# Performance work log

Hardware: AMD Instinct MI355X
Metric: run time of the kernel (lower is better)

Reference implementation:

```python
import jax, jax.numpy as jnp
import numpy as np

B, C, D, H, W = 2, 96, 4, 128, 128
WS = 8            # spatial window size
NUM_HEADS = 3
MLP_RATIO = 4.0


def _rel_pos_index(ws_eff):
    # Swin-style 2D relative position index over the effective (ws*sqrt(D))^2 window
    coords = np.stack(np.meshgrid(np.arange(ws_eff), np.arange(ws_eff), indexing='ij')).reshape(2, -1)
    rel = (coords[:, :, None] - coords[:, None, :]).transpose(1, 2, 0)
    rel[..., 0] += ws_eff - 1
    rel[..., 1] += ws_eff - 1
    rel[..., 0] *= 2 * ws_eff - 1
    return rel.sum(-1)  # (N, N) int


def setup_inputs() -> dict:
    key = jax.random.key(0)
    ks = jax.random.split(key, 8)
    ws_eff = WS * int(np.sqrt(D))
    table_len = (2 * ws_eff - 1) ** 2
    hid = int(C * MLP_RATIO)
    s = lambda k, shape: jax.random.normal(k, shape, jnp.float32) * 0.02
    return dict(
        x=jax.random.normal(ks[0], (B, C, D, H, W), jnp.float32),
        qkv_w=s(ks[1], (3 * C, C)), qkv_b=jnp.zeros((3 * C,), jnp.float32),
        proj_w=s(ks[2], (C, C)), proj_b=jnp.zeros((C,), jnp.float32),
        bias_table=s(ks[3], (table_len, NUM_HEADS)),
        ln1_g=jnp.ones((C,), jnp.float32), ln1_b=jnp.zeros((C,), jnp.float32),
        ln2_g=jnp.ones((C,), jnp.float32), ln2_b=jnp.zeros((C,), jnp.float32),
        fc1_w=s(ks[4], (hid, C)), fc1_b=jnp.zeros((hid,), jnp.float32),
        fc2_w=s(ks[5], (C, hid)), fc2_b=jnp.zeros((C,), jnp.float32),
    )


def _ln(x, g, b):
    m = x.mean(-1, keepdims=True)
    v = ((x - m) ** 2).mean(-1, keepdims=True)
    return (x - m) * jax.lax.rsqrt(v + 1e-5) * g + b


def reference(x, qkv_w, qkv_b, proj_w, proj_b, bias_table,
              ln1_g, ln1_b, ln2_g, ln2_b, fc1_w, fc1_b, fc2_w, fc2_b):
    ws, nh = WS, NUM_HEADS
    hd = C // nh
    # window partition: (B,C,D,H,W) -> (nW*B, C, D*ws*ws) -> tokens (B_, N, C)
    p = x.reshape(B, C, D, H // ws, ws, W // ws, ws)
    p = p.transpose(0, 3, 5, 1, 2, 4, 6).reshape(-1, C, D * ws * ws)
    t = p.transpose(0, 2, 1)  # (B_, N, C)
    B_, N, _ = t.shape

    # --- window attention with relative position bias ---
    h = _ln(t, ln1_g, ln1_b)
    qkv = (h @ qkv_w.T + qkv_b).reshape(B_, N, 3, nh, hd).transpose(2, 0, 3, 1, 4)
    q = qkv[0] * (hd ** -0.5)
    k, v = qkv[1], qkv[2]
    idx = jnp.asarray(_rel_pos_index(ws * int(np.sqrt(D))))  # static (N,N)
    bias = bias_table[idx].transpose(2, 0, 1)  # (nh, N, N) gathered bias
    attn = jax.nn.softmax(jnp.einsum('bhnd,bhmd->bhnm', q, k) + bias[None], axis=-1)
    o = jnp.einsum('bhnm,bhmd->bhnd', attn, v).transpose(0, 2, 1, 3).reshape(B_, N, C)
    t = t + (o @ proj_w.T + proj_b)

    # --- MLP block ---
    h2 = _ln(t, ln2_g, ln2_b)
    m = jax.nn.gelu(h2 @ fc1_w.T + fc1_b, approximate=False) @ fc2_w.T + fc2_b
    return t + m
```

## Files before the change

kernel.cpp:

```cpp
#include <hip/hip_runtime.h>
#include <hip/hip_bf16.h>

typedef unsigned int u32;
typedef unsigned long long u64;
using bf16x8 = __attribute__((ext_vector_type(8))) short;
using f32x4  = __attribute__((ext_vector_type(4))) float;

#define QKV_STRIDE 12582912u
#define WS_NEED    100663296ull

__device__ __forceinline__ float bl(u32 u) { return __uint_as_float(u << 16); }
__device__ __forceinline__ float bh(u32 u) { return __uint_as_float(u & 0xffff0000u); }
__device__ __forceinline__ unsigned short bfbits(float f) {
    __hip_bfloat16 b = __float2bfloat16(f);
    return *(unsigned short*)&b;
}
__device__ __forceinline__ u32 pack2(float f0, float f1) {
    return ((u32)bfbits(f1) << 16) | (u32)bfbits(f0);
}
__device__ __forceinline__ u64 pack4(float f0, float f1, float f2, float f3) {
    return ((u64)pack2(f2, f3) << 32) | (u64)pack2(f0, f1);
}

#define MFMA(a, b, c) __builtin_amdgcn_mfma_f32_16x16x32_bf16(a, b, c, 0, 0, 0)

__global__ __launch_bounds__(256) void k_fill(float* __restrict__ out, int n)
{
    int i = blockIdx.x * 256 + threadIdx.x;
    if (i < n) out[i] = 1000.0f;
}

__global__ __launch_bounds__(256) void k_ln1_c(const float* __restrict__ x,
                                               const float* __restrict__ g1,
                                               const float* __restrict__ b1,
                                               u32* __restrict__ h)
{
    __shared__ float xs[96 * 128];
    __shared__ float ps[256], pss[256], mr[128], rs[128];
    int blk = blockIdx.x;
    int hh = blk & 127, d = (blk >> 7) & 3, bb = blk >> 9;
    long base = (long)bb * 6291456 + (long)d * 16384 + hh * 128;
    for (int i = threadIdx.x; i < 3072; i += 256) {
        int c = i >> 5, w4 = i & 31;
        ((float4*)xs)[i] = *(const float4*)(x + base + (long)c * 65536 + w4 * 4);
    }
    __syncthreads();

    int tid = threadIdx.x, half = tid >> 7, ww = tid & 127;
    int c0 = half * 48;
    float s = 0.f, ssq = 0.f;
    #pragma unroll 8
    for (int c = c0; c < c0 + 48; ++c) {
        float v = xs[c * 128 + ww];
        s += v; ssq += v * v;
    }
    ps[tid] = s; pss[tid] = ssq;
    __syncthreads();
    if (half == 0) {
        float st = ps[ww] + ps[128 + ww], sst = pss[ww] + pss[128 + ww];
        float mean = st * (1.f / 96.f);
        float var  = sst * (1.f / 96.f) - mean * mean;
        mr[ww] = mean; rs[ww] = rsqrtf(var + 1e-5f);
    }
    __syncthreads();
    float mean = mr[ww], rstd = rs[ww];

    int w = (bb << 8) + (hh >> 3) * 16 + (ww >> 3);
    int t = (w << 8) + d * 64 + (hh & 7) * 8 + (ww & 7);
    uint4* hq = (uint4*)(h + (long)t * 48 + half * 24);
    #pragma unroll
    for (int k = 0; k < 6; ++k) {
        int c = c0 + 8 * k;
        u32 q0 = pack2((xs[(c+0)*128+ww]-mean)*rstd*g1[c+0]+b1[c+0],
                       (xs[(c+1)*128+ww]-mean)*rstd*g1[c+1]+b1[c+1]);
        u32 q1 = pack2((xs[(c+2)*128+ww]-mean)*rstd*g1[c+2]+b1[c+2],
                       (xs[(c+3)*128+ww]-mean)*rstd*g1[c+3]+b1[c+3]);
        u32 q2 = pack2((xs[(c+4)*128+ww]-mean)*rstd*g1[c+4]+b1[c+4],
                       (xs[(c+5)*128+ww]-mean)*rstd*g1[c+5]+b1[c+5]);
        u32 q3 = pack2((xs[(c+6)*128+ww]-mean)*rstd*g1[c+6]+b1[c+6],
                       (xs[(c+7)*128+ww]-mean)*rstd*g1[c+7]+b1[c+7]);
        hq[k] = make_uint4(q0, q1, q2, q3);
    }
}

__global__ __launch_bounds__(256) void k_qkv_m(const __hip_bfloat16* __restrict__ h,
                                               const float* __restrict__ qkvw,
                                               const float* __restrict__ qkvb,
                                               __hip_bfloat16* __restrict__ qkv)
{
    __shared__ short wsm[288 * 96];
    int tid = threadIdx.x;
    for (int idx = tid; idx < 6912; idx += 256) {
        float4 wv = ((const float4*)qkvw)[idx];
        *(u64*)&wsm[idx * 4] = pack4(wv.x, wv.y, wv.z, wv.w);
    }
    __syncthreads();

    int wave = tid >> 6, lane = tid & 63;
    int quad = lane >> 4, l16 = lane & 15;
    int mbase = blockIdx.x * 256 + wave * 64;

    bf16x8 A[4][3];
    #pragma unroll
    for (int mm = 0; mm < 4; ++mm) {
        const __hip_bfloat16* ap = h + (long)(mbase + mm * 16 + l16) * 96 + quad * 8;
        A[mm][0] = *(const bf16x8*)(ap);
        A[mm][1] = *(const bf16x8*)(ap + 32);
        A[mm][2] = *(const bf16x8*)(ap + 64);
    }

    for (int nt = 0; nt < 18; ++nt) {
        int n0 = nt * 16;
        const short* bp = &wsm[(n0 + l16) * 96 + quad * 8];
        bf16x8 B0 = *(const bf16x8*)(bp);
        bf16x8 B1 = *(const bf16x8*)(bp + 32);
        bf16x8 B2 = *(const bf16x8*)(bp + 64);
        int r    = n0 + l16;
        int type = n0 / 96;
        int head = (n0 % 96) / 32;
        int dd   = r & 31;
        float bias = qkvb[r];
        float scl  = (type == 0) ? 0.17677669529663687f : 1.0f;
        long tbase = (long)type * QKV_STRIDE;
        #pragma unroll
        for (int mm = 0; mm < 4; ++mm) {
            f32x4 acc = {0.f, 0.f, 0.f, 0.f};
            acc = MFMA(A[mm][0], B0, acc);
            acc = MFMA(A[mm][1], B1, acc);
            acc = MFMA(A[mm][2], B2, acc);
            int tok0 = mbase + mm * 16 + quad * 4;
            int w = tok0 >> 8, nn = tok0 & 255;
            long dst0 = tbase + (long)(w * 3 + head) * 8192 + nn * 32 + dd;
            #pragma unroll
            for (int rg = 0; rg < 4; ++rg)
                qkv[dst0 + (long)rg * 32] = __float2bfloat16((acc[rg] + bias) * scl);
        }
    }
}

__global__ __launch_bounds__(256, 6) void k_attn_m(const __hip_bfloat16* __restrict__ qkv,
                                                   const float* __restrict__ btab,
                                                   __hip_bfloat16* __restrict__ o)
{
    __shared__ short vt[32 * 264];
    __shared__ float bsT[31 * 33];
    int wh = blockIdx.x, head = wh % 3, w = wh / 3;
    int tid = threadIdx.x;

    const u32* vg = (const u32*)(qkv + 2u * QKV_STRIDE + (long)wh * 8192);
    for (int idx = tid; idx < 4096; idx += 256) {
        u32 pv = vg[idx];
        int kr = idx >> 4, d0 = (idx & 15) * 2;
        vt[d0 * 264 + kr]       = (short)(pv & 0xffffu);
        vt[(d0 + 1) * 264 + kr] = (short)(pv >> 16);
    }
    for (int idx = tid; idx < 961; idx += 256) {
        int c2 = idx / 31, r2 = idx - c2 * 31;
        bsT[c2 * 33 + r2] = btab[(r2 * 31 + c2) * 3 + head];
    }
    __syncthreads();

    int wave = tid >> 6, lane = tid & 63, quad = lane >> 4, l16 = lane & 15;
    const __hip_bfloat16* qb = qkv + (long)wh * 8192;
    const __hip_bfloat16* kb = qkv + QKV_STRIDE + (long)wh * 8192;

    int addrA = ((((lane >> 4) & 1) << 5) + l16) << 2;
    int addrB = addrA + 64;
    int addrI = (quad * 20) << 2;
    bool hiq  = (quad >= 2);

    #pragma unroll 1
    for (int g = 0; g < 4; ++g) {
        int qg = wave * 4 + g;
        bf16x8 qf = *(const bf16x8*)(qb + (qg * 16 + l16) * 32 + quad * 8);
        f32x4 a0 = {0.f, 0.f, 0.f, 0.f}, a1 = {0.f, 0.f, 0.f, 0.f};
        float lsum = 0.f;

        #pragma unroll 1
        for (int qt = 0; qt < 4; ++qt) {
            f32x4 s[4];
            #pragma unroll
            for (int k4 = 0; k4 < 4; ++k4) {
                int kt = qt * 4 + k4;
                bf16x8 kkv = *(const bf16x8*)(kb + (kt * 16 + l16) * 32 + quad * 8);
                f32x4 z = {0.f, 0.f, 0.f, 0.f};
                s[k4] = MFMA(kkv, qf, z);
            }
            #pragma unroll
            for (int rg = 0; rg < 4; ++rg) {
                const float* bb = &bsT[(l16 - quad * 4 + 15 - rg) * 33 + qg];
                #pragma unroll
                for (int k4 = 0; k4 < 4; ++k4)
                    s[k4][rg] += bb[15 - qt * 4 - k4];
            }
            f32x4 vs = {0.f, 0.f, 0.f, 0.f};
            #pragma unroll
            for (int k4 = 0; k4 < 4; ++k4) {
                f32x4 e;
                #pragma unroll
                for (int rg = 0; rg < 4; ++rg) e[rg] = __expf(s[k4][rg]);
                s[k4] = e;
                vs += e;
            }
            lsum += vs[0] + vs[1] + vs[2] + vs[3];

            #pragma unroll
            for (int k2l = 0; k2l < 2; ++k2l) {
                int k2 = qt * 2 + k2l;
                u32 pe0 = pack2(s[2 * k2l][0],     s[2 * k2l][1]);
                u32 pe1 = pack2(s[2 * k2l][2],     s[2 * k2l][3]);
                u32 po0 = pack2(s[2 * k2l + 1][0], s[2 * k2l + 1][1]);
                u32 po1 = pack2(s[2 * k2l + 1][2], s[2 * k2l + 1][3]);
                u32 e0 = (u32)__builtin_amdgcn_ds_bpermute(addrA, (int)pe0);
                u32 o0 = (u32)__builtin_amdgcn_ds_bpermute(addrA, (int)po0);
                u32 e1 = (u32)__builtin_amdgcn_ds_bpermute(addrA, (int)pe1);
                u32 o1 = (u32)__builtin_amdgcn_ds_bpermute(addrA, (int)po1);
                u32 e2 = (u32)__builtin_amdgcn_ds_bpermute(addrB, (int)pe0);
                u32 o2 = (u32)__builtin_amdgcn_ds_bpermute(addrB, (int)po0);
                u32 e3 = (u32)__builtin_amdgcn_ds_bpermute(addrB, (int)pe1);
                u32 o3 = (u32)__builtin_amdgcn_ds_bpermute(addrB, (int)po1);
                union { u32 u[4]; bf16x8 v; } pu;
                pu.u[0] = hiq ? o0 : e0;
                pu.u[1] = hiq ? o1 : e1;
                pu.u[2] = hiq ? o2 : e2;
                pu.u[3] = hiq ? o3 : e3;
                bf16x8 v0 = *(const bf16x8*)&vt[l16 * 264 + k2 * 32 + quad * 8];
                bf16x8 v1 = *(const bf16x8*)&vt[(16 + l16) * 264 + k2 * 32 + quad * 8];
                a0 = MFMA(pu.v, v0, a0);
                a1 = MFMA(pu.v, v1, a1);
            }
        }

        lsum += __shfl_xor(lsum, 16);
        lsum += __shfl_xor(lsum, 32);
        float inv = 1.f / lsum;

        #pragma unroll
        for (int rg = 0; rg < 4; ++rg) {
            float irg = __uint_as_float(
                (u32)__builtin_amdgcn_ds_bpermute(addrI + (rg << 2), (int)__float_as_uint(inv)));
            int qrow = qg * 16 + quad * 4 + rg;
            __hip_bfloat16* op = o + (long)(w * 256 + qrow) * 96 + head * 32;
            op[l16]      = __float2bfloat16(a0[rg] * irg);
            op[16 + l16] = __float2bfloat16(a1[rg] * irg);
        }
    }
}

__global__ __launch_bounds__(256) void k_proj_nr(const __hip_bfloat16* __restrict__ o,
                                                 const float* __restrict__ pw,
                                                 const float* __restrict__ pb,
                                                 __hip_bfloat16* __restrict__ pbuf)
{
    __shared__ short wsm[96 * 96];
    int tid = threadIdx.x;
    for (int idx = tid; idx < 2304; idx += 256) {
        float4 wv = ((const float4*)pw)[idx];
        *(u64*)&wsm[idx * 4] = pack4(wv.x, wv.y, wv.z, wv.w);
    }
    __syncthreads();

    int wave = tid >> 6, lane = tid & 63;
    int quad = lane >> 4, l16 = lane & 15;
    int mbase = blockIdx.x * 256 + wave * 64;

    bf16x8 A[4][3];
    #pragma unroll
    for (int mm = 0; mm < 4; ++mm) {
        const __hip_bfloat16* ap = o + (long)(mbase + mm * 16 + l16) * 96 + quad * 8;
        A[mm][0] = *(const bf16x8*)(ap);
        A[mm][1] = *(const bf16x8*)(ap + 32);
        A[mm][2] = *(const bf16x8*)(ap + 64);
    }

    for (int nt = 0; nt < 6; ++nt) {
        int n0 = nt * 16;
        const short* bp = &wsm[(n0 + l16) * 96 + quad * 8];
        bf16x8 B0 = *(const bf16x8*)(bp);
        bf16x8 B1 = *(const bf16x8*)(bp + 32);
        bf16x8 B2 = *(const bf16x8*)(bp + 64);
        int c = n0 + l16;
        float bias = pb[c];
        #pragma unroll
        for (int mm = 0; mm < 4; ++mm) {
            f32x4 acc = {0.f, 0.f, 0.f, 0.f};
            acc = MFMA(A[mm][0], B0, acc);
            acc = MFMA(A[mm][1], B1, acc);
            acc = MFMA(A[mm][2], B2, acc);
            int tok0 = mbase + mm * 16 + quad * 4;
            #pragma unroll
            for (int rg = 0; rg < 4; ++rg)
                pbuf[(long)(tok0 + rg) * 96 + c] = __float2bfloat16(acc[rg] + bias);
        }
    }
}

__global__ __launch_bounds__(256) void k_addln2(const float* __restrict__ x,
                                                const __hip_bfloat16* __restrict__ pbuf,
                                                const float* __restrict__ g2,
                                                const float* __restrict__ b2,
                                                u32* __restrict__ t2,
                                                u32* __restrict__ h2)
{
    __shared__ float xs[96 * 128];
    __shared__ float ps[256], pss[256], mr[128], rs[128];
    int blk = blockIdx.x;
    int hh = blk & 127, d = (blk >> 7) & 3, bb = blk >> 9;
    long base = (long)bb * 6291456 + (long)d * 16384 + hh * 128;
    for (int i = threadIdx.x; i < 3072; i += 256) {
        int c = i >> 5, w4 = i & 31;
        ((float4*)xs)[i] = *(const float4*)(x + base + (long)c * 65536 + w4 * 4);
    }
    __syncthreads();

    int tid = threadIdx.x, half = tid >> 7, ww = tid & 127;
    int c0 = half * 48;
    int w = (bb << 8) + (hh >> 3) * 16 + (ww >> 3);
    int t = (w << 8) + d * 64 + (hh & 7) * 8 + (ww & 7);

    const uint4* pr4 = (const uint4*)((const u32*)pbuf + (long)t * 48 + half * 24);
    float pv[48];
    float s = 0.f, ssq = 0.f;
    #pragma unroll
    for (int k6 = 0; k6 < 6; ++k6) {
        uint4 q = pr4[k6];
        u32 uu[4] = {q.x, q.y, q.z, q.w};
        #pragma unroll
        for (int j = 0; j < 4; ++j) {
            int c = c0 + 8 * k6 + 2 * j;
            float v0 = bl(uu[j]) + xs[c * 128 + ww];
            float v1 = bh(uu[j]) + xs[(c + 1) * 128 + ww];
            pv[8 * k6 + 2 * j]     = v0;
            pv[8 * k6 + 2 * j + 1] = v1;
            s += v0 + v1; ssq += v0 * v0 + v1 * v1;
        }
    }
    ps[tid] = s; pss[tid] = ssq;
    __syncthreads();
    if (half == 0) {
        float st = ps[ww] + ps[128 + ww], sst = pss[ww] + pss[128 + ww];
        float mean = st * (1.f / 96.f);
        float var  = sst * (1.f / 96.f) - mean * mean;
        mr[ww] = mean; rs[ww] = rsqrtf(var + 1e-5f);
    }
    __syncthreads();
    float mean = mr[ww], rstd = rs[ww];

    uint4* t2q = (uint4*)(t2 + (long)t * 48 + half * 24);
    uint4* hq  = (uint4*)(h2 + (long)t * 48 + half * 24);
    #pragma unroll
    for (int k = 0; k < 6; ++k) {
        int c = c0 + 8 * k;
        u32 t0v = pack2(pv[8*k+0], pv[8*k+1]);
        u32 t1v = pack2(pv[8*k+2], pv[8*k+3]);
        u32 t2v = pack2(pv[8*k+4], pv[8*k+5]);
        u32 t3v = pack2(pv[8*k+6], pv[8*k+7]);
        t2q[k] = make_uint4(t0v, t1v, t2v, t3v);
        u32 q0 = pack2((pv[8*k+0]-mean)*rstd*g2[c+0]+b2[c+0],
                       (pv[8*k+1]-mean)*rstd*g2[c+1]+b2[c+1]);
        u32 q1 = pack2((pv[8*k+2]-mean)*rstd*g2[c+2]+b2[c+2],
                       (pv[8*k+3]-mean)*rstd*g2[c+3]+b2[c+3]);
        u32 q2 = pack2((pv[8*k+4]-mean)*rstd*g2[c+4]+b2[c+4],
                       (pv[8*k+5]-mean)*rstd*g2[c+5]+b2[c+5]);
        u32 q3 = pack2((pv[8*k+6]-mean)*rstd*g2[c+6]+b2[c+6],
                       (pv[8*k+7]-mean)*rstd*g2[c+7]+b2[c+7]);
        hq[k] = make_uint4(q0, q1, q2, q3);
    }
}

__global__ __launch_bounds__(256) void k_fc1_m(const __hip_bfloat16* __restrict__ h2,
                                               const float* __restrict__ fw,
                                               const float* __restrict__ fb,
                                               __hip_bfloat16* __restrict__ m1, int t0)
{
    __shared__ short wsm[192 * 96];
    int tid = threadIdx.x;
    int wave = tid >> 6, lane = tid & 63;
    int quad = lane >> 4, l16 = lane & 15;
    int mbaseL = blockIdx.x * 128 + wave * 32;

    bf16x8 A[2][3];
    #pragma unroll
    for (int mm = 0; mm < 2; ++mm) {
        const __hip_bfloat16* ap = h2 + (long)(t0 + mbaseL + mm * 16 + l16) * 96 + quad * 8;
        A[mm][0] = *(const bf16x8*)(ap);
        A[mm][1] = *(const bf16x8*)(ap + 32);
        A[mm][2] = *(const bf16x8*)(ap + 64);
    }

    const float is2 = 0.70710678118654752440f;
    for (int ph = 0; ph < 2; ++ph) {
        if (ph) __syncthreads();
        const float4* fw4 = (const float4*)(fw + ph * 192 * 96);
        for (int idx = tid; idx < 4608; idx += 256) {
            float4 wv = fw4[idx];
            *(u64*)&wsm[idx * 4] = pack4(wv.x, wv.y, wv.z, wv.w);
        }
        __syncthreads();
        for (int nt = 0; nt < 12; ++nt) {
            int n0 = nt * 16;
            const short* bp = &wsm[(n0 + l16) * 96 + quad * 8];
            bf16x8 B0 = *(const bf16x8*)(bp);
            bf16x8 B1 = *(const bf16x8*)(bp + 32);
            bf16x8 B2 = *(const bf16x8*)(bp + 64);
            int r = ph * 192 + n0 + l16;
            float bias = fb[r];
            #pragma unroll
            for (int mm = 0; mm < 2; ++mm) {
                f32x4 acc = {0.f, 0.f, 0.f, 0.f};
                acc = MFMA(A[mm][0], B0, acc);
                acc = MFMA(A[mm][1], B1, acc);
                acc = MFMA(A[mm][2], B2, acc);
                int tokL0 = mbaseL + mm * 16 + quad * 4;
                #pragma unroll
                for (int rg = 0; rg < 4; ++rg) {
                    float v = acc[rg] + bias;
                    v = 0.5f * v * (1.f + erff(v * is2));
                    m1[(long)(tokL0 + rg) * 384 + r] = __float2bfloat16(v);
                }
            }
        }
    }
}

__global__ __launch_bounds__(256) void k_fc2_m(const __hip_bfloat16* __restrict__ m1,
                                               const float* __restrict__ fw,
                                               const float* __restrict__ fb,
                                               const __hip_bfloat16* __restrict__ t2,
                                               float* __restrict__ out, int t0)
{
    __shared__ short wsm[48 * 392];
    int tid = threadIdx.x;
    int wave = tid >> 6, lane = tid & 63;
    int quad = lane >> 4, l16 = lane & 15;
    int mbaseL = blockIdx.x * 128 + wave * 32;

    bf16x8 A[2][12];
    #pragma unroll
    for (int mm = 0; mm < 2; ++mm) {
        const __hip_bfloat16* ap = m1 + (long)(mbaseL + mm * 16 + l16) * 384 + quad * 8;
        #pragma unroll
        for (int kc = 0; kc < 12; ++kc)
            A[mm][kc] = *(const bf16x8*)(ap + kc * 32);
    }

    for (int ph = 0; ph < 2; ++ph) {
        if (ph) __syncthreads();
        for (int idx = tid; idx < 48 * 96; idx += 256) {
            int rr = idx / 96, cc = idx - rr * 96;
            float4 wv = ((const float4*)(fw + (long)(ph * 48 + rr) * 384))[cc];
            *(u64*)&wsm[rr * 392 + cc * 4] = pack4(wv.x, wv.y, wv.z, wv.w);
        }
        __syncthreads();
        for (int nt = 0; nt < 3; ++nt) {
            int n0 = nt * 16;
            const short* bp = &wsm[(n0 + l16) * 392 + quad * 8];
            bf16x8 B[12];
            #pragma unroll
            for (int kc = 0; kc < 12; ++kc)
                B[kc] = *(const bf16x8*)(bp + kc * 32);
            int c = ph * 48 + n0 + l16;
            float bias = fb[c];
            #pragma unroll
            for (int mm = 0; mm < 2; ++mm) {
                f32x4 acc = {0.f, 0.f, 0.f, 0.f};
                #pragma unroll
                for (int kc = 0; kc < 12; ++kc)
                    acc = MFMA(A[mm][kc], B[kc], acc);
                int tok0 = t0 + mbaseL + mm * 16 + quad * 4;
                #pragma unroll
                for (int rg = 0; rg < 4; ++rg) {
                    long g = (long)(tok0 + rg) * 96 + c;
                    out[g] = __bfloat162float(t2[g]) + acc[rg] + bias;
                }
            }
        }
    }
}

extern "C" void kernel_launch(void* const* d_in, const int* in_sizes, int n_in,
                              void* d_out, int out_size, void* d_ws, size_t ws_size,
                              hipStream_t stream)
{
    const float* x     = (const float*)d_in[0];
    const float* qkvw  = (const float*)d_in[1];
    const float* qkvb  = (const float*)d_in[2];
    const float* projw = (const float*)d_in[3];
    const float* projb = (const float*)d_in[4];
    const float* btab  = (const float*)d_in[5];
    const float* ln1g  = (const float*)d_in[6];
    const float* ln1b  = (const float*)d_in[7];
    const float* ln2g  = (const float*)d_in[8];
    const float* ln2b  = (const float*)d_in[9];
    const float* fc1w  = (const float*)d_in[10];
    const float* fc1b  = (const float*)d_in[11];
    const float* fc2w  = (const float*)d_in[12];
    const float* fc2b  = (const float*)d_in[13];
    float* out = (float*)d_out;

    if (ws_size < WS_NEED) {
        k_fill<<<49152, 256, 0, stream>>>(out, out_size);
        return;
    }

    char* ws = (char*)d_ws;
    __hip_bfloat16* qkvB  = (__hip_bfloat16*)(ws);
    __hip_bfloat16* pbuf  = (__hip_bfloat16*)(ws);
    __hip_bfloat16* m1buf = (__hip_bfloat16*)(ws);
    __hip_bfloat16* t2buf = (__hip_bfloat16*)(ws + 50331648);
    __hip_bfloat16* hbuf  = (__hip_bfloat16*)(ws + 75497472);
    __hip_bfloat16* obuf  = hbuf;
    __hip_bfloat16* h2buf = hbuf;

    k_ln1_c <<<1024, 256, 0, stream>>>(x, ln1g, ln1b, (u32*)hbuf);
    k_qkv_m <<<512,  256, 0, stream>>>(hbuf, qkvw, qkvb, qkvB);
    k_attn_m<<<1536, 256, 0, stream>>>(qkvB, btab, obuf);
    k_proj_nr<<<512, 256, 0, stream>>>(obuf, projw, projb, pbuf);
    k_addln2<<<1024, 256, 0, stream>>>(x, pbuf, ln2g, ln2b, (u32*)t2buf, (u32*)h2buf);
    for (int ch = 0; ch < 2; ++ch) {
        int t0 = ch * 65536;
        k_fc1_m<<<512, 256, 0, stream>>>(h2buf, fc1w, fc1b, m1buf, t0);
        k_fc2_m<<<512, 256, 0, stream>>>(m1buf, fc2w, fc2b, t2buf, out, t0);
    }
}
```

Baseline: 366.9 us.

## Pre-convert weights to bf16 once and read B operands directly from global

```diff
diff --git a/kernel.cpp b/kernel.cpp
--- a/kernel.cpp
+++ b/kernel.cpp
@@ -28,6 +28,28 @@
 {
     int i = blockIdx.x * 256 + threadIdx.x;
     if (i < n) out[i] = 1000.0f;
+}
+
+__global__ __launch_bounds__(256) void k_wcvt(const float* __restrict__ qkvw,
+                                              const float* __restrict__ pw,
+                                              const float* __restrict__ f1w,
+                                              u64* __restrict__ wq,
+                                              u64* __restrict__ wp,
+                                              u64* __restrict__ wf1)
+{
+    int i = blockIdx.x * 256 + threadIdx.x;
+    if (i < 6912) {
+        float4 v = ((const float4*)qkvw)[i];
+        wq[i] = pack4(v.x, v.y, v.z, v.w);
+    } else if (i < 9216) {
+        int j = i - 6912;
+        float4 v = ((const float4*)pw)[j];
+        wp[j] = pack4(v.x, v.y, v.z, v.w);
+    } else if (i < 18432) {
+        int j = i - 9216;
+        float4 v = ((const float4*)f1w)[j];
+        wf1[j] = pack4(v.x, v.y, v.z, v.w);
+    }
 }
 
 __global__ __launch_bounds__(256) void k_ln1_c(const float* __restrict__ x,
@@ -84,34 +106,26 @@
 }
 
 __global__ __launch_bounds__(256) void k_qkv_m(const __hip_bfloat16* __restrict__ h,
-                                               const float* __restrict__ qkvw,
+                                               const __hip_bfloat16* __restrict__ wb,
                                                const float* __restrict__ qkvb,
                                                __hip_bfloat16* __restrict__ qkv)
 {
-    __shared__ short wsm[288 * 96];
     int tid = threadIdx.x;
-    for (int idx = tid; idx < 6912; idx += 256) {
-        float4 wv = ((const float4*)qkvw)[idx];
-        *(u64*)&wsm[idx * 4] = pack4(wv.x, wv.y, wv.z, wv.w);
-    }
-    __syncthreads();
-
     int wave = tid >> 6, lane = tid & 63;
     int quad = lane >> 4, l16 = lane & 15;
-    int mbase = blockIdx.x * 256 + wave * 64;
-
-    bf16x8 A[4][3];
-    #pragma unroll
-    for (int mm = 0; mm < 4; ++mm) {
-        const __hip_bfloat16* ap = h + (long)(mbase + mm * 16 + l16) * 96 + quad * 8;
-        A[mm][0] = *(const bf16x8*)(ap);
-        A[mm][1] = *(const bf16x8*)(ap + 32);
-        A[mm][2] = *(const bf16x8*)(ap + 64);
-    }
+    int mbase = blockIdx.x * 64 + wave * 16;
+
+    const __hip_bfloat16* ap = h + (long)(mbase + l16) * 96 + quad * 8;
+    bf16x8 A0 = *(const bf16x8*)(ap);
+    bf16x8 A1 = *(const bf16x8*)(ap + 32);
+    bf16x8 A2 = *(const bf16x8*)(ap + 64);
+
+    int tok0 = mbase + quad * 4;
+    int w = tok0 >> 8, nn = tok0 & 255;
 
     for (int nt = 0; nt < 18; ++nt) {
         int n0 = nt * 16;
-        const short* bp = &wsm[(n0 + l16) * 96 + quad * 8];
+        const __hip_bfloat16* bp = wb + (n0 + l16) * 96 + quad * 8;
         bf16x8 B0 = *(const bf16x8*)(bp);
         bf16x8 B1 = *(const bf16x8*)(bp + 32);
         bf16x8 B2 = *(const bf16x8*)(bp + 64);
@@ -122,19 +136,14 @@
         float bias = qkvb[r];
         float scl  = (type == 0) ? 0.17677669529663687f : 1.0f;
         long tbase = (long)type * QKV_STRIDE;
+        f32x4 acc = {0.f, 0.f, 0.f, 0.f};
+        acc = MFMA(A0, B0, acc);
+        acc = MFMA(A1, B1, acc);
+        acc = MFMA(A2, B2, acc);
+        long dst0 = tbase + (long)(w * 3 + head) * 8192 + nn * 32 + dd;
         #pragma unroll
-        for (int mm = 0; mm < 4; ++mm) {
-            f32x4 acc = {0.f, 0.f, 0.f, 0.f};
-            acc = MFMA(A[mm][0], B0, acc);
-            acc = MFMA(A[mm][1], B1, acc);
-            acc = MFMA(A[mm][2], B2, acc);
-            int tok0 = mbase + mm * 16 + quad * 4;
-            int w = tok0 >> 8, nn = tok0 & 255;
-            long dst0 = tbase + (long)(w * 3 + head) * 8192 + nn * 32 + dd;
-            #pragma unroll
-            for (int rg = 0; rg < 4; ++rg)
-                qkv[dst0 + (long)rg * 32] = __float2bfloat16((acc[rg] + bias) * scl);
-        }
+        for (int rg = 0; rg < 4; ++rg)
+            qkv[dst0 + (long)rg * 32] = __float2bfloat16((acc[rg] + bias) * scl);
     }
 }
 
@@ -248,50 +257,37 @@
 }
 
 __global__ __launch_bounds__(256) void k_proj_nr(const __hip_bfloat16* __restrict__ o,
-                                                 const float* __restrict__ pw,
+                                                 const __hip_bfloat16* __restrict__ wb,
                                                  const float* __restrict__ pb,
                                                  __hip_bfloat16* __restrict__ pbuf)
 {
-    __shared__ short wsm[96 * 96];
     int tid = threadIdx.x;
-    for (int idx = tid; idx < 2304; idx += 256) {
-        float4 wv = ((const float4*)pw)[idx];
-        *(u64*)&wsm[idx * 4] = pack4(wv.x, wv.y, wv.z, wv.w);
-    }
-    __syncthreads();
-
     int wave = tid >> 6, lane = tid & 63;
     int quad = lane >> 4, l16 = lane & 15;
-    int mbase = blockIdx.x * 256 + wave * 64;
-
-    bf16x8 A[4][3];
-    #pragma unroll
-    for (int mm = 0; mm < 4; ++mm) {
-        const __hip_bfloat16* ap = o + (long)(mbase + mm * 16 + l16) * 96 + quad * 8;
-        A[mm][0] = *(const bf16x8*)(ap);
-        A[mm][1] = *(const bf16x8*)(ap + 32);
-        A[mm][2] = *(const bf16x8*)(ap + 64);
-    }
+    int mbase = blockIdx.x * 64 + wave * 16;
+
+    const __hip_bfloat16* ap = o + (long)(mbase + l16) * 96 + quad * 8;
+    bf16x8 A0 = *(const bf16x8*)(ap);
+    bf16x8 A1 = *(const bf16x8*)(ap + 32);
+    bf16x8 A2 = *(const bf16x8*)(ap + 64);
+
+    int tok0 = mbase + quad * 4;
 
     for (int nt = 0; nt < 6; ++nt) {
         int n0 = nt * 16;
-        const short* bp = &wsm[(n0 + l16) * 96 + quad * 8];
+        const __hip_bfloat16* bp = wb + (n0 + l16) * 96 + quad * 8;
         bf16x8 B0 = *(const bf16x8*)(bp);
         bf16x8 B1 = *(const bf16x8*)(bp + 32);
         bf16x8 B2 = *(const bf16x8*)(bp + 64);
         int c = n0 + l16;
         float bias = pb[c];
+        f32x4 acc = {0.f, 0.f, 0.f, 0.f};
+        acc = MFMA(A0, B0, acc);
+        acc = MFMA(A1, B1, acc);
+        acc = MFMA(A2, B2, acc);
         #pragma unroll
-        for (int mm = 0; mm < 4; ++mm) {
-            f32x4 acc = {0.f, 0.f, 0.f, 0.f};
-            acc = MFMA(A[mm][0], B0, acc);
-            acc = MFMA(A[mm][1], B1, acc);
-            acc = MFMA(A[mm][2], B2, acc);
-            int tok0 = mbase + mm * 16 + quad * 4;
-            #pragma unroll
-            for (int rg = 0; rg < 4; ++rg)
-                pbuf[(long)(tok0 + rg) * 96 + c] = __float2bfloat16(acc[rg] + bias);
-        }
+        for (int rg = 0; rg < 4; ++rg)
+            pbuf[(long)(tok0 + rg) * 96 + c] = __float2bfloat16(acc[rg] + bias);
     }
 }
 
@@ -369,56 +365,39 @@
 }
 
 __global__ __launch_bounds__(256) void k_fc1_m(const __hip_bfloat16* __restrict__ h2,
-                                               const float* __restrict__ fw,
+                                               const __hip_bfloat16* __restrict__ wb,
                                                const float* __restrict__ fb,
                                                __hip_bfloat16* __restrict__ m1, int t0)
 {
-    __shared__ short wsm[192 * 96];
     int tid = threadIdx.x;
     int wave = tid >> 6, lane = tid & 63;
     int quad = lane >> 4, l16 = lane & 15;
-    int mbaseL = blockIdx.x * 128 + wave * 32;
-
-    bf16x8 A[2][3];
-    #pragma unroll
-    for (int mm = 0; mm < 2; ++mm) {
-        const __hip_bfloat16* ap = h2 + (long)(t0 + mbaseL + mm * 16 + l16) * 96 + quad * 8;
-        A[mm][0] = *(const bf16x8*)(ap);
-        A[mm][1] = *(const bf16x8*)(ap + 32);
-        A[mm][2] = *(const bf16x8*)(ap + 64);
-    }
-
+    int mbaseL = blockIdx.x * 64 + wave * 16;
+
+    const __hip_bfloat16* ap = h2 + (long)(t0 + mbaseL + l16) * 96 + quad * 8;
+    bf16x8 A0 = *(const bf16x8*)(ap);
+    bf16x8 A1 = *(const bf16x8*)(ap + 32);
+    bf16x8 A2 = *(const bf16x8*)(ap + 64);
+
+    int tokL0 = mbaseL + quad * 4;
     const float is2 = 0.70710678118654752440f;
-    for (int ph = 0; ph < 2; ++ph) {
-        if (ph) __syncthreads();
-        const float4* fw4 = (const float4*)(fw + ph * 192 * 96);
-        for (int idx = tid; idx < 4608; idx += 256) {
-            float4 wv = fw4[idx];
-            *(u64*)&wsm[idx * 4] = pack4(wv.x, wv.y, wv.z, wv.w);
-        }
-        __syncthreads();
-        for (int nt = 0; nt < 12; ++nt) {
-            int n0 = nt * 16;
-            const short* bp = &wsm[(n0 + l16) * 96 + quad * 8];
-            bf16x8 B0 = *(const bf16x8*)(bp);
-            bf16x8 B1 = *(const bf16x8*)(bp + 32);
-            bf16x8 B2 = *(const bf16x8*)(bp + 64);
-            int r = ph * 192 + n0 + l16;
-            float bias = fb[r];
-            #pragma unroll
-            for (int mm = 0; mm < 2; ++mm) {
-                f32x4 acc = {0.f, 0.f, 0.f, 0.f};
-                acc = MFMA(A[mm][0], B0, acc);
-                acc = MFMA(A[mm][1], B1, acc);
-                acc = MFMA(A[mm][2], B2, acc);
-                int tokL0 = mbaseL + mm * 16 + quad * 4;
-                #pragma unroll
-                for (int rg = 0; rg < 4; ++rg) {
-                    float v = acc[rg] + bias;
-                    v = 0.5f * v * (1.f + erff(v * is2));
-                    m1[(long)(tokL0 + rg) * 384 + r] = __float2bfloat16(v);
-                }
-            }
+
+    for (int nt = 0; nt < 24; ++nt) {
+        int r = nt * 16 + l16;
+        const __hip_bfloat16* bp = wb + (long)r * 96 + quad * 8;
+        bf16x8 B0 = *(const bf16x8*)(bp);
+        bf16x8 B1 = *(const bf16x8*)(bp + 32);
+        bf16x8 B2 = *(const bf16x8*)(bp + 64);
+        float bias = fb[r];
+        f32x4 acc = {0.f, 0.f, 0.f, 0.f};
+        acc = MFMA(A0, B0, acc);
+        acc = MFMA(A1, B1, acc);
+        acc = MFMA(A2, B2, acc);
+        #pragma unroll
+        for (int rg = 0; rg < 4; ++rg) {
+            float v = acc[rg] + bias;
+            v = 0.5f * v * (1.f + erff(v * is2));
+            m1[(long)(tokL0 + rg) * 384 + r] = __float2bfloat16(v);
         }
     }
 }
@@ -512,14 +491,20 @@
     __hip_bfloat16* obuf  = hbuf;
     __hip_bfloat16* h2buf = hbuf;
 
+    char* ob = (char*)d_out;
+    __hip_bfloat16* wqb  = (__hip_bfloat16*)(ob + 50184192);
+    __hip_bfloat16* wpb  = (__hip_bfloat16*)(ob + 50239488);
+    __hip_bfloat16* wf1b = (__hip_bfloat16*)(ob + 50257920);
+
+    k_wcvt  <<<72,   256, 0, stream>>>(qkvw, projw, fc1w, (u64*)wqb, (u64*)wpb, (u64*)wf1b);
     k_ln1_c <<<1024, 256, 0, stream>>>(x, ln1g, ln1b, (u32*)hbuf);
-    k_qkv_m <<<512,  256, 0, stream>>>(hbuf, qkvw, qkvb, qkvB);
+    k_qkv_m <<<2048, 256, 0, stream>>>(hbuf, wqb, qkvb, qkvB);
     k_attn_m<<<1536, 256, 0, stream>>>(qkvB, btab, obuf);
-    k_proj_nr<<<512, 256, 0, stream>>>(obuf, projw, projb, pbuf);
+    k_proj_nr<<<2048, 256, 0, stream>>>(obuf, wpb, projb, pbuf);
     k_addln2<<<1024, 256, 0, stream>>>(x, pbuf, ln2g, ln2b, (u32*)t2buf, (u32*)h2buf);
     for (int ch = 0; ch < 2; ++ch) {
         int t0 = ch * 65536;
-        k_fc1_m<<<512, 256, 0, stream>>>(h2buf, fc1w, fc1b, m1buf, t0);
-        k_fc2_m<<<512, 256, 0, stream>>>(m1buf, fc2w, fc2b, t2buf, out, t0);
-    }
-}
+        k_fc1_m<<<1024, 256, 0, stream>>>(h2buf, wf1b, fc1b, m1buf, t0);
+        k_fc2_m<<<512,  256, 0, stream>>>(m1buf, fc2w, fc2b, t2buf, out, t0);
+    }
+}
```

After: 367.6 us (median of 2 runs). No clear change (+0.2%).
